# Optimization experiments

Measured on AMD Instinct MI355X. Metric: run time of the kernel, lower is better.

Reference implementation:

```python
import jax, jax.numpy as jnp
import numpy as np

B, N, C_IN = 8, 2048, 64
NUM_TERMS, NUM_CHANNELS = 3, 64
LN_EPS = 1e-5


def setup_inputs() -> dict:
    key = jax.random.key(0)
    k1, k2, k3 = jax.random.split(key, 3)
    A = jax.random.normal(k1, (B, N, N), dtype=jnp.float32) / jnp.sqrt(N).astype(jnp.float32)
    X = jax.random.normal(k2, (B, N, C_IN), dtype=jnp.float32)
    # xavier_uniform on h of shape [num_terms+1, num_channels, num_nodes]
    fan_in, fan_out = NUM_CHANNELS, N
    bound = float(np.sqrt(6.0 / (fan_in + fan_out)))
    h = jax.random.uniform(k3, (NUM_TERMS + 1, NUM_CHANNELS, N), dtype=jnp.float32,
                           minval=-bound, maxval=bound)
    gamma = jnp.ones((NUM_CHANNELS,), dtype=jnp.float32)
    beta = jnp.zeros((NUM_CHANNELS,), dtype=jnp.float32)
    return {"A": A, "X": X, "h": h, "gamma": gamma, "beta": beta}


def reference(A, X, h, gamma, beta):
    # Original loops compute: Y[b,n,c] = sum_i h[i,c,n] * (A^i @ sum_ch X[...,ch])[b,n]
    num_terms = h.shape[0] - 1
    Xs = X.sum(axis=-1)  # [B, N] -- inner channel loop collapses to a sum

    def step(p, _):
        p_next = jnp.einsum('bmn,bn->bm', A, p)  # A^i @ Xs
        return p_next, p_next

    _, Ps = jax.lax.scan(step, Xs, None, length=num_terms)  # [T, B, N]
    P = jnp.concatenate([Xs[None], Ps], axis=0)  # [T+1, B, N], P[0] = I @ Xs

    Y = jnp.einsum('icn,ibn->bnc', h, P)  # [B, N, C]

    mean = Y.mean(axis=-1, keepdims=True)
    var = Y.var(axis=-1, keepdims=True)
    Yn = (Y - mean) * jax.lax.rsqrt(var + LN_EPS) * gamma + beta
    return jnp.tanh(Yn)
```

## Files before the change

### kernel.cpp

```cpp
#include <hip/hip_runtime.h>
#include <hip/hip_fp16.h>
#include <math.h>

#define BB 8
#define NN 2048
#define NCH 64
#define LN_EPS 1e-5f
#define BN (BB * NN)

typedef float f4 __attribute__((ext_vector_type(4)));

__global__ __launch_bounds__(256, 4) void xsum_kernel(
        const float* __restrict__ X, float* __restrict__ P) {
    const int tid = threadIdx.x;
    const int row = blockIdx.x * 16 + (tid >> 4);
    const int q   = tid & 15;
    float4 x = ((const float4*)X)[(size_t)row * 16 + q];
    float v = x.x + x.y + x.z + x.w;
    v += __shfl_xor(v, 8, 64);
    v += __shfl_xor(v, 4, 64);
    v += __shfl_xor(v, 2, 64);
    v += __shfl_xor(v, 1, 64);
    if (q == 0) P[row] = v;
}

__global__ __launch_bounds__(256, 4) void matvec_cvt_kernel(
        const float* __restrict__ A,
        const float* __restrict__ pin,
        float* __restrict__ pout,
        __half* __restrict__ A16) {
    __shared__ float4 p4[NN / 4];
    const int tid  = threadIdx.x;
    const int wave = tid >> 6;
    const int lane = tid & 63;
    const int b    = blockIdx.y;
    const int m0   = blockIdx.x * 16 + wave * 4;
    const float* Ab = A + (size_t)b * NN * NN;

    f4 buf[2][8];
    {
        const f4* r = (const f4*)(Ab + (size_t)m0 * NN);
        #pragma unroll
        for (int j = 0; j < 8; ++j)
            buf[0][j] = __builtin_nontemporal_load(&r[j * 64 + lane]);
    }
    const float4* src = (const float4*)(pin + (size_t)b * NN);
    p4[tid]       = src[tid];
    p4[tid + 256] = src[tid + 256];
    __syncthreads();

    #pragma unroll
    for (int i = 0; i < 4; ++i) {
        const int m = m0 + i;
        if (i < 3) {
            const f4* rn = (const f4*)(Ab + (size_t)(m + 1) * NN);
            #pragma unroll
            for (int j = 0; j < 8; ++j)
                buf[(i + 1) & 1][j] = __builtin_nontemporal_load(&rn[j * 64 + lane]);
        }
        float acc = 0.f;
        #pragma unroll
        for (int j = 0; j < 8; ++j) {
            f4 x      = buf[i & 1][j];
            float4 pv = p4[j * 64 + lane];
            acc += x.x * pv.x + x.y * pv.y + x.z * pv.z + x.w * pv.w;
        }
        float2* A16r = (float2*)(A16 + (size_t)b * NN * NN + (size_t)m * NN);
        #pragma unroll
        for (int j = 0; j < 8; ++j) {
            union { float2 f2; __half2 h2[2]; } u;
            u.h2[0] = __floats2half2_rn(buf[i & 1][j].x, buf[i & 1][j].y);
            u.h2[1] = __floats2half2_rn(buf[i & 1][j].z, buf[i & 1][j].w);
            A16r[j * 64 + lane] = u.f2;
        }
        #pragma unroll
        for (int off = 32; off > 0; off >>= 1)
            acc += __shfl_down(acc, off, 64);
        if (lane == 0) pout[(size_t)b * NN + m] = acc;
    }
}

__global__ __launch_bounds__(256, 8) void matvec16_kernel(
        const __half* __restrict__ A16,
        const float* __restrict__ pin,
        float* __restrict__ pout) {
    __shared__ float4 p4[NN / 4];
    const int tid  = threadIdx.x;
    const int wave = tid >> 6;
    const int lane = tid & 63;
    const int b    = blockIdx.y;
    const int m0   = blockIdx.x * 8 + wave * 2;
    const __half* Ab = A16 + (size_t)b * NN * NN;

    float4 buf[2][4];
    #pragma unroll
    for (int r = 0; r < 2; ++r) {
        const float4* rr = (const float4*)(Ab + (size_t)(m0 + r) * NN);
        #pragma unroll
        for (int j = 0; j < 4; ++j) buf[r][j] = rr[j * 64 + lane];
    }
    const float4* src = (const float4*)(pin + (size_t)b * NN);
    p4[tid]       = src[tid];
    p4[tid + 256] = src[tid + 256];
    __syncthreads();

    #pragma unroll
    for (int r = 0; r < 2; ++r) {
        const int m = m0 + r;
        float acc = 0.f;
        #pragma unroll
        for (int j = 0; j < 4; ++j) {
            float4 pa = p4[2 * (j * 64 + lane)];
            float4 pb = p4[2 * (j * 64 + lane) + 1];
            const __half2* hx = (const __half2*)&buf[r][j];
            float2 f0 = __half22float2(hx[0]);
            float2 f1 = __half22float2(hx[1]);
            float2 f2 = __half22float2(hx[2]);
            float2 f3 = __half22float2(hx[3]);
            acc += f0.x * pa.x + f0.y * pa.y + f1.x * pa.z + f1.y * pa.w
                 + f2.x * pb.x + f2.y * pb.y + f3.x * pb.z + f3.y * pb.w;
        }
        #pragma unroll
        for (int off = 32; off > 0; off >>= 1)
            acc += __shfl_down(acc, off, 64);
        if (lane == 0) pout[(size_t)b * NN + m] = acc;
    }
}

__global__ __launch_bounds__(256, 4) void matvec16_ln_kernel(
        const __half* __restrict__ A16,
        const float* __restrict__ P,
        const float* __restrict__ h,
        const float* __restrict__ gamma,
        const float* __restrict__ beta,
        float* __restrict__ out) {
    __shared__ float4 p4[NN / 4];
    __shared__ float  hs[8][NCH][4];
    const int tid  = threadIdx.x;
    const int wave = tid >> 6;
    const int lane = tid & 63;
    const int b    = blockIdx.y;
    const int bx   = blockIdx.x;
    const int m0   = bx * 8 + wave * 2;
    const __half* Ab = A16 + (size_t)b * NN * NN;

    float4 buf[2][4];
    #pragma unroll
    for (int r = 0; r < 2; ++r) {
        const float4* rr = (const float4*)(Ab + (size_t)(m0 + r) * NN);
        #pragma unroll
        for (int j = 0; j < 4; ++j) buf[r][j] = rr[j * 64 + lane];
    }

    {
        const float4* src = (const float4*)(P + (size_t)(2 * BB + b) * NN);
        p4[tid]       = src[tid];
        p4[tid + 256] = src[tid + 256];
    }
    {
        const float4* hr =
            (const float4*)(h + ((size_t)(wave * NCH + lane)) * NN + bx * 8);
        #pragma unroll
        for (int k = 0; k < 2; ++k) {
            float4 hv = hr[k];
            hs[k * 4 + 0][lane][wave] = hv.x;
            hs[k * 4 + 1][lane][wave] = hv.y;
            hs[k * 4 + 2][lane][wave] = hv.z;
            hs[k * 4 + 3][lane][wave] = hv.w;
        }
    }
    __syncthreads();

    const float g  = gamma[lane];
    const float be = beta[lane];

    #pragma unroll
    for (int r = 0; r < 2; ++r) {
        const int m   = m0 + r;
        const int idx = b * NN + m;
        const float p0 = P[idx];
        const float p1 = P[BN + idx];

        float acc = 0.f;
        #pragma unroll
        for (int j = 0; j < 4; ++j) {
            float4 pa = p4[2 * (j * 64 + lane)];
            float4 pb = p4[2 * (j * 64 + lane) + 1];
            const __half2* hx = (const __half2*)&buf[r][j];
            float2 f0 = __half22float2(hx[0]);
            float2 f1 = __half22float2(hx[1]);
            float2 f2 = __half22float2(hx[2]);
            float2 f3 = __half22float2(hx[3]);
            acc += f0.x * pa.x + f0.y * pa.y + f1.x * pa.z + f1.y * pa.w
                 + f2.x * pb.x + f2.y * pb.y + f3.x * pb.z + f3.y * pb.w;
        }
        #pragma unroll
        for (int off = 32; off > 0; off >>= 1)
            acc += __shfl_xor(acc, off, 64);
        const float p3 = acc;
        const float p2 = ((const float*)p4)[m];

        const int  node = wave * 2 + r;
        const float4 hv = *(const float4*)&hs[node][lane][0];
        float y = hv.x * p0 + hv.y * p1 + hv.z * p2 + hv.w * p3;

        float sum = y;
        #pragma unroll
        for (int off = 32; off > 0; off >>= 1)
            sum += __shfl_xor(sum, off, 64);
        const float mean = sum * (1.f / NCH);

        float d  = y - mean;
        float vs = d * d;
        #pragma unroll
        for (int off = 32; off > 0; off >>= 1)
            vs += __shfl_xor(vs, off, 64);
        const float rstd = rsqrtf(vs * (1.f / NCH) + LN_EPS);

        __builtin_nontemporal_store(
            tanhf(d * rstd * g + be),
            &out[(size_t)idx * NCH + lane]);
    }
}

extern "C" void kernel_launch(void* const* d_in, const int* in_sizes, int n_in,
                              void* d_out, int out_size, void* d_ws, size_t ws_size,
                              hipStream_t stream) {
    const float* A     = (const float*)d_in[0];
    const float* X     = (const float*)d_in[1];
    const float* h     = (const float*)d_in[2];
    const float* gamma = (const float*)d_in[3];
    const float* beta  = (const float*)d_in[4];
    float* out = (float*)d_out;

    float*  P   = (float*)d_ws;
    __half* A16 = (__half*)((char*)d_ws + (1u << 20));

    xsum_kernel<<<dim3(BN / 16), dim3(256), 0, stream>>>(X, P);

    matvec_cvt_kernel<<<dim3(NN / 16, BB), dim3(256), 0, stream>>>(
        A, P, P + BN, A16);

    matvec16_kernel<<<dim3(NN / 8, BB), dim3(256), 0, stream>>>(
        A16, P + BN, P + 2 * BN);

    matvec16_ln_kernel<<<dim3(NN / 8, BB), dim3(256), 0, stream>>>(
        A16, P, h, gamma, beta, out);
}
```

Baseline: 227.7 us.

## Drop fp16 copy of A and reread fp32 A through cache

Removes the fp16 shadow copy of A that the first matvec pass wrote and the later passes read. All three matvec passes now read the original fp32 A with ordinary loads instead of nontemporal ones, so the 128MB matrix can stay resident in the large last-level cache between passes. This avoids the 64MB fp16 write and the half-to-float conversions, and restores full fp32 precision. The cost is more bytes read per later pass and larger per-thread register buffers, which can lower occupancy.

```diff
diff --git a/kernel.cpp b/kernel.cpp
--- a/kernel.cpp
+++ b/kernel.cpp
@@ -1,5 +1,4 @@
 #include <hip/hip_runtime.h>
-#include <hip/hip_fp16.h>
 #include <math.h>
 
 #define BB 8
@@ -9,6 +8,7 @@
 #define BN (BB * NN)
 
 typedef float f4 __attribute__((ext_vector_type(4)));
+
 
 __global__ __launch_bounds__(256, 4) void xsum_kernel(
         const float* __restrict__ X, float* __restrict__ P) {
@@ -24,11 +24,10 @@
     if (q == 0) P[row] = v;
 }
 
-__global__ __launch_bounds__(256, 4) void matvec_cvt_kernel(
+__global__ __launch_bounds__(256, 4) void matvec_kernel_a(
         const float* __restrict__ A,
         const float* __restrict__ pin,
-        float* __restrict__ pout,
-        __half* __restrict__ A16) {
+        float* __restrict__ pout) {
     __shared__ float4 p4[NN / 4];
     const int tid  = threadIdx.x;
     const int wave = tid >> 6;
@@ -42,7 +41,7 @@
         const f4* r = (const f4*)(Ab + (size_t)m0 * NN);
         #pragma unroll
         for (int j = 0; j < 8; ++j)
-            buf[0][j] = __builtin_nontemporal_load(&r[j * 64 + lane]);
+            buf[0][j] = r[j * 64 + lane];
     }
     const float4* src = (const float4*)(pin + (size_t)b * NN);
     p4[tid]       = src[tid];
@@ -56,7 +55,7 @@
             const f4* rn = (const f4*)(Ab + (size_t)(m + 1) * NN);
             #pragma unroll
             for (int j = 0; j < 8; ++j)
-                buf[(i + 1) & 1][j] = __builtin_nontemporal_load(&rn[j * 64 + lane]);
+                buf[(i + 1) & 1][j] = rn[j * 64 + lane];
         }
         float acc = 0.f;
         #pragma unroll
@@ -65,14 +64,6 @@
             float4 pv = p4[j * 64 + lane];
             acc += x.x * pv.x + x.y * pv.y + x.z * pv.z + x.w * pv.w;
         }
-        float2* A16r = (float2*)(A16 + (size_t)b * NN * NN + (size_t)m * NN);
-        #pragma unroll
-        for (int j = 0; j < 8; ++j) {
-            union { float2 f2; __half2 h2[2]; } u;
-            u.h2[0] = __floats2half2_rn(buf[i & 1][j].x, buf[i & 1][j].y);
-            u.h2[1] = __floats2half2_rn(buf[i & 1][j].z, buf[i & 1][j].w);
-            A16r[j * 64 + lane] = u.f2;
-        }
         #pragma unroll
         for (int off = 32; off > 0; off >>= 1)
             acc += __shfl_down(acc, off, 64);
@@ -80,8 +71,8 @@
     }
 }
 
-__global__ __launch_bounds__(256, 8) void matvec16_kernel(
-        const __half* __restrict__ A16,
+__global__ __launch_bounds__(256, 4) void matvec_kernel_b(
+        const float* __restrict__ A,
         const float* __restrict__ pin,
         float* __restrict__ pout) {
     __shared__ float4 p4[NN / 4];
@@ -90,14 +81,14 @@
     const int lane = tid & 63;
     const int b    = blockIdx.y;
     const int m0   = blockIdx.x * 8 + wave * 2;
-    const __half* Ab = A16 + (size_t)b * NN * NN;
-
-    float4 buf[2][4];
-    #pragma unroll
-    for (int r = 0; r < 2; ++r) {
-        const float4* rr = (const float4*)(Ab + (size_t)(m0 + r) * NN);
-        #pragma unroll
-        for (int j = 0; j < 4; ++j) buf[r][j] = rr[j * 64 + lane];
+    const float* Ab = A + (size_t)b * NN * NN;
+
+    f4 buf[2][8];
+    #pragma unroll
+    for (int r = 0; r < 2; ++r) {
+        const f4* rr = (const f4*)(Ab + (size_t)(m0 + r) * NN);
+        #pragma unroll
+        for (int j = 0; j < 8; ++j) buf[r][j] = rr[j * 64 + lane];
     }
     const float4* src = (const float4*)(pin + (size_t)b * NN);
     p4[tid]       = src[tid];
@@ -109,16 +100,10 @@
         const int m = m0 + r;
         float acc = 0.f;
         #pragma unroll
-        for (int j = 0; j < 4; ++j) {
-            float4 pa = p4[2 * (j * 64 + lane)];
-            float4 pb = p4[2 * (j * 64 + lane) + 1];
-            const __half2* hx = (const __half2*)&buf[r][j];
-            float2 f0 = __half22float2(hx[0]);
-            float2 f1 = __half22float2(hx[1]);
-            float2 f2 = __half22float2(hx[2]);
-            float2 f3 = __half22float2(hx[3]);
-            acc += f0.x * pa.x + f0.y * pa.y + f1.x * pa.z + f1.y * pa.w
-                 + f2.x * pb.x + f2.y * pb.y + f3.x * pb.z + f3.y * pb.w;
+        for (int j = 0; j < 8; ++j) {
+            f4 x      = buf[r][j];
+            float4 pv = p4[j * 64 + lane];
+            acc += x.x * pv.x + x.y * pv.y + x.z * pv.z + x.w * pv.w;
         }
         #pragma unroll
         for (int off = 32; off > 0; off >>= 1)
@@ -127,8 +112,8 @@
     }
 }
 
-__global__ __launch_bounds__(256, 4) void matvec16_ln_kernel(
-        const __half* __restrict__ A16,
+__global__ __launch_bounds__(256, 4) void matvec_ln_kernel(
+        const float* __restrict__ A,
         const float* __restrict__ P,
         const float* __restrict__ h,
         const float* __restrict__ gamma,
@@ -142,14 +127,14 @@
     const int b    = blockIdx.y;
     const int bx   = blockIdx.x;
     const int m0   = bx * 8 + wave * 2;
-    const __half* Ab = A16 + (size_t)b * NN * NN;
-
-    float4 buf[2][4];
-    #pragma unroll
-    for (int r = 0; r < 2; ++r) {
-        const float4* rr = (const float4*)(Ab + (size_t)(m0 + r) * NN);
-        #pragma unroll
-        for (int j = 0; j < 4; ++j) buf[r][j] = rr[j * 64 + lane];
+    const float* Ab = A + (size_t)b * NN * NN;
+
+    f4 buf[2][8];
+    #pragma unroll
+    for (int r = 0; r < 2; ++r) {
+        const f4* rr = (const f4*)(Ab + (size_t)(m0 + r) * NN);
+        #pragma unroll
+        for (int j = 0; j < 8; ++j) buf[r][j] = rr[j * 64 + lane];
     }
 
     {
@@ -183,16 +168,10 @@
 
         float acc = 0.f;
         #pragma unroll
-        for (int j = 0; j < 4; ++j) {
-            float4 pa = p4[2 * (j * 64 + lane)];
-            float4 pb = p4[2 * (j * 64 + lane) + 1];
-            const __half2* hx = (const __half2*)&buf[r][j];
-            float2 f0 = __half22float2(hx[0]);
-            float2 f1 = __half22float2(hx[1]);
-            float2 f2 = __half22float2(hx[2]);
-            float2 f3 = __half22float2(hx[3]);
-            acc += f0.x * pa.x + f0.y * pa.y + f1.x * pa.z + f1.y * pa.w
-                 + f2.x * pb.x + f2.y * pb.y + f3.x * pb.z + f3.y * pb.w;
+        for (int j = 0; j < 8; ++j) {
+            f4 x      = buf[r][j];
+            float4 pv = p4[j * 64 + lane];
+            acc += x.x * pv.x + x.y * pv.y + x.z * pv.z + x.w * pv.w;
         }
         #pragma unroll
         for (int off = 32; off > 0; off >>= 1)
@@ -233,17 +212,16 @@
     const float* beta  = (const float*)d_in[4];
     float* out = (float*)d_out;
 
-    float*  P   = (float*)d_ws;
-    __half* A16 = (__half*)((char*)d_ws + (1u << 20));
+    float* P = (float*)d_ws;
 
     xsum_kernel<<<dim3(BN / 16), dim3(256), 0, stream>>>(X, P);
 
-    matvec_cvt_kernel<<<dim3(NN / 16, BB), dim3(256), 0, stream>>>(
-        A, P, P + BN, A16);
-
-    matvec16_kernel<<<dim3(NN / 8, BB), dim3(256), 0, stream>>>(
-        A16, P + BN, P + 2 * BN);
-
-    matvec16_ln_kernel<<<dim3(NN / 8, BB), dim3(256), 0, stream>>>(
-        A16, P, h, gamma, beta, out);
-}
+    matvec_kernel_a<<<dim3(NN / 16, BB), dim3(256), 0, stream>>>(
+        A, P, P + BN);
+
+    matvec_kernel_b<<<dim3(NN / 8, BB), dim3(256), 0, stream>>>(
+        A, P + BN, P + 2 * BN);
+
+    matvec_ln_kernel<<<dim3(NN / 8, BB), dim3(256), 0, stream>>>(
+        A, P, h, gamma, beta, out);
+}
```

After: 243.1 us. +6.7%, slower.
